# Optimization experiments

Measured on AMD Instinct MI355X. Metric: run time of the kernel, lower is better.

The kernel has to match this reference:

```python
import jax, jax.numpy as jnp
import numpy as np

N = 100000      # nodes
E = 1600000     # edges (avg degree 16)
IN = 128        # in_size
H = 4           # num_heads
DH = 16         # hid_size (per-head)
DO = 16         # out_size (per-head)
NEG_SLOPE = 0.2 # DGL GATConv default leaky_relu slope


def setup_inputs():
    key = jax.random.key(0)
    ks = jax.random.split(key, 12)
    s = 0.1
    return {
        "x":   jax.random.normal(ks[0], (N, IN), jnp.float32),
        "src": jax.random.randint(ks[1], (E,), 0, N, jnp.int32),
        "dst": jax.random.randint(ks[2], (E,), 0, N, jnp.int32),
        # layer 1: in=128 -> H*DH=64, residual Linear (128 != 64)
        "W1":    jax.random.normal(ks[3], (IN, H * DH), jnp.float32) * s,
        "al1":   jax.random.normal(ks[4], (H, DH), jnp.float32) * s,
        "ar1":   jax.random.normal(ks[5], (H, DH), jnp.float32) * s,
        "resW1": jax.random.normal(ks[6], (IN, H * DH), jnp.float32) * s,
        "b1":    jnp.zeros((H * DH,), jnp.float32),
        # layer 2: in=H*DH=64 -> H*DO=64, residual is Identity reshape (64 == 64)
        "W2":  jax.random.normal(ks[7], (H * DH, H * DO), jnp.float32) * s,
        "al2": jax.random.normal(ks[8], (H, DO), jnp.float32) * s,
        "ar2": jax.random.normal(ks[9], (H, DO), jnp.float32) * s,
        "b2":  jnp.zeros((H * DO,), jnp.float32),
    }


def gat_layer(h, W, al, ar, res, bias, src, dst):
    """One DGL-style GATConv (no internal activation). Returns [N, H, D]."""
    d = W.shape[1] // H
    feat = (h @ W).reshape(-1, H, d)                       # [N,H,D]
    el = jnp.einsum('nhd,hd->nh', feat, al)                # [N,H]
    er = jnp.einsum('nhd,hd->nh', feat, ar)                # [N,H]
    e = jax.nn.leaky_relu(el[src] + er[dst], NEG_SLOPE)    # [E,H]
    # segment softmax over incoming edges of each destination node
    emax = jax.lax.stop_gradient(jax.ops.segment_max(e, dst, num_segments=N))
    ee = jnp.exp(e - emax[dst])                            # [E,H]
    den = jax.ops.segment_sum(ee, dst, num_segments=N)     # [N,H]
    alpha = ee / den[dst]                                  # [E,H]
    msg = alpha[:, :, None] * feat[src]                    # [E,H,D]
    out = jax.ops.segment_sum(msg, dst, num_segments=N)    # [N,H,D]
    return out + res + bias.reshape(1, H, d)


def reference(x, src, dst, W1, al1, ar1, resW1, b1, W2, al2, ar2, b2):
    # layer 1 (residual via Linear since IN != H*DH)
    res1 = (x @ resW1).reshape(N, H, DH)
    h = gat_layer(x, W1, al1, ar1, res1, b1, src, dst)     # [N,H,DH]
    h = jax.nn.elu(h.reshape(N, H * DH))                   # flatten + elu (dropout=eval identity)
    # layer 2 (identity residual since H*DH == H*DO)
    res2 = h.reshape(N, H, DO)
    h = gat_layer(h, W2, al2, ar2, res2, b2, src, dst)     # [N,H,DO]
    return h.mean(axis=1)                                  # [N,DO]
```

## Files before the change

kernel.cpp:

```cpp
#include <hip/hip_runtime.h>
#include <hip/hip_bf16.h>

static inline int cdiv(int a, int b){ return (a+b-1)/b; }

#define LEAKY(x) ((x) >= 0.f ? (x) : 0.2f*(x))

#define NBK   256
#define NBKSH 8
#define CAP   5120
#define SCAP  1024

__device__ inline unsigned short bf16bits(float f){
  __hip_bfloat16 h = __float2bfloat16(f);
  return *reinterpret_cast<unsigned short*>(&h);
}


__global__ __launch_bounds__(256) void binA(const int* __restrict__ src,
    const int* __restrict__ dst, int* __restrict__ acur, unsigned int* __restrict__ tmp,
    int E, int B, int epb)
{
  __shared__ int cnt1[512], cnt2[512], gbase[512];
  const int tid = threadIdx.x;
  for (int j = tid; j < 512; j += 256) { cnt1[j] = 0; cnt2[j] = 0; }
  __syncthreads();
  const int beg = blockIdx.x*epb, end = min(E, beg+epb);
  for (int e = beg+tid; e < end; e += 256) atomicAdd(&cnt1[dst[e]>>NBKSH], 1);
  __syncthreads();
  for (int j = tid; j < B; j += 256) gbase[j] = atomicAdd(&acur[j], cnt1[j]);
  __syncthreads();
  for (int e = beg+tid; e < end; e += 256) {
    int s = src[e], d = dst[e];
    int b = d >> NBKSH;
    int tk = atomicAdd(&cnt2[b], 1);
    int slot = gbase[b] + tk;
    if (slot < CAP)
      tmp[(size_t)b*CAP + slot] = ((unsigned)s << NBKSH) | (unsigned)(d & (NBK-1));
  }
}


__global__ __launch_bounds__(512) void bucket_scan(const int* __restrict__ acur,
    int* __restrict__ bbase, int* __restrict__ off, int B, int N, int E)
{
  __shared__ int wsum[8];
  const int tid = threadIdx.x, lane = tid & 63, wave = tid >> 6;
  int v = (tid < B) ? acur[tid] : 0;
  int x = v;
  #pragma unroll
  for (int s = 1; s < 64; s <<= 1) { int t = __shfl_up(x, s); if (lane >= s) x += t; }
  if (lane == 63) wsum[wave] = x;
  __syncthreads();
  if (tid == 0) { int r = 0; for (int w = 0; w < 8; w++) { int t = wsum[w]; wsum[w] = r; r += t; } }
  __syncthreads();
  int excl = wsum[wave] + x - v;
  if (tid < B)    bbase[tid] = excl;
  if (tid == B-1) bbase[B]   = excl + v;
  if (tid == 0)   off[N]     = E;
}


__global__ __launch_bounds__(256) void binC(const unsigned int* __restrict__ tmp,
    const int* __restrict__ acur, const int* __restrict__ bbase,
    int* __restrict__ off, int* __restrict__ csr_src, int N)
{
  __shared__ int sA[NBK], sB[NBK];
  const int b = blockIdx.x, tid = threadIdx.x;
  const int m = min(acur[b], CAP);
  const int base = bbase[b];
  const int n0 = b*NBK;
  const int nn = min(NBK, N - n0);
  if (tid < NBK) sA[tid] = 0;
  __syncthreads();
  const unsigned int* tb = tmp + (size_t)b*CAP;
  for (int i = tid; i < m; i += 256) atomicAdd(&sA[tb[i] & (NBK-1)], 1);
  __syncthreads();
  int* in = sA; int* ob = sB;
  for (int st = 1; st < NBK; st <<= 1) {
    if (tid < NBK) { int v = in[tid]; if (tid >= st) v += in[tid-st]; ob[tid] = v; }
    __syncthreads();
    int* t = in; in = ob; ob = t;
  }
  if (tid < NBK) ob[tid] = tid ? in[tid-1] : 0;
  __syncthreads();
  if (tid < nn) off[n0 + tid] = base + ob[tid];
  __syncthreads();
  for (int i = tid; i < m; i += 256) {
    unsigned v = tb[i];
    int pos = atomicAdd(&ob[v & (NBK-1)], 1);
    csr_src[base + pos] = (int)(v >> NBKSH);
  }
}


__global__ __launch_bounds__(256) void lin128_once(const float* __restrict__ X,
    const float* __restrict__ W, const float* __restrict__ RW,
    const float* __restrict__ al, const float* __restrict__ ar,
    unsigned short* __restrict__ featb, float* __restrict__ el, float* __restrict__ er,
    float* __restrict__ res, int n)
{
  __shared__ float Ws[128*64];
  __shared__ float Xs[32*129];
  const int tid = threadIdx.x;
  const int nbase = blockIdx.x * 32;
  for (int i = tid; i < 128*64/4; i += 256) ((float4*)Ws)[i] = ((const float4*)W)[i];
  for (int idx = tid; idx < 32*32; idx += 256) {
    int node = idx >> 5, fq = idx & 31;
    int gn = nbase + node;
    float4 v = (gn < n) ? ((const float4*)X)[(size_t)gn*32 + fq] : float4{0.f,0.f,0.f,0.f};
    Xs[node*129 + fq*4 + 0] = v.x;
    Xs[node*129 + fq*4 + 1] = v.y;
    Xs[node*129 + fq*4 + 2] = v.z;
    Xs[node*129 + fq*4 + 3] = v.w;
  }
  __syncthreads();
  const int c0 = (tid & 15) * 4;
  const int n0 = (tid >> 4) * 2;
  const int g0 = nbase + n0, g1 = g0 + 1;
  {
    float a00=0,a01=0,a02=0,a03=0, a10=0,a11=0,a12=0,a13=0;
    #pragma unroll 4
    for (int k = 0; k < 128; k++) {
      float4 w = *(const float4*)&Ws[k*64 + c0];
      float x0 = Xs[n0*129 + k];
      float x1 = Xs[n0*129 + 129 + k];
      a00 = fmaf(x0, w.x, a00); a01 = fmaf(x0, w.y, a01);
      a02 = fmaf(x0, w.z, a02); a03 = fmaf(x0, w.w, a03);
      a10 = fmaf(x1, w.x, a10); a11 = fmaf(x1, w.y, a11);
      a12 = fmaf(x1, w.z, a12); a13 = fmaf(x1, w.w, a13);
    }
    if (g0 < n) *(ushort4*)&featb[(size_t)g0*64 + c0] = ushort4{bf16bits(a00),bf16bits(a01),bf16bits(a02),bf16bits(a03)};
    if (g1 < n) *(ushort4*)&featb[(size_t)g1*64 + c0] = ushort4{bf16bits(a10),bf16bits(a11),bf16bits(a12),bf16bits(a13)};
    float l0=al[c0], l1=al[c0+1], l2=al[c0+2], l3=al[c0+3];
    float r0=ar[c0], r1=ar[c0+1], r2=ar[c0+2], r3=ar[c0+3];
    float e0 = a00*l0 + a01*l1 + a02*l2 + a03*l3;
    float e1 = a10*l0 + a11*l1 + a12*l2 + a13*l3;
    float q0 = a00*r0 + a01*r1 + a02*r2 + a03*r3;
    float q1 = a10*r0 + a11*r1 + a12*r2 + a13*r3;
    e0 += __shfl_xor(e0,1); e0 += __shfl_xor(e0,2);
    e1 += __shfl_xor(e1,1); e1 += __shfl_xor(e1,2);
    q0 += __shfl_xor(q0,1); q0 += __shfl_xor(q0,2);
    q1 += __shfl_xor(q1,1); q1 += __shfl_xor(q1,2);
    if ((tid & 3) == 0) {
      int h = (tid & 15) >> 2;
      if (g0 < n) { el[g0*4+h] = e0; er[g0*4+h] = q0; }
      if (g1 < n) { el[g1*4+h] = e1; er[g1*4+h] = q1; }
    }
  }
  __syncthreads();
  for (int i = tid; i < 128*64/4; i += 256) ((float4*)Ws)[i] = ((const float4*)RW)[i];
  __syncthreads();
  {
    float a00=0,a01=0,a02=0,a03=0, a10=0,a11=0,a12=0,a13=0;
    #pragma unroll 4
    for (int k = 0; k < 128; k++) {
      float4 w = *(const float4*)&Ws[k*64 + c0];
      float x0 = Xs[n0*129 + k];
      float x1 = Xs[n0*129 + 129 + k];
      a00 = fmaf(x0, w.x, a00); a01 = fmaf(x0, w.y, a01);
      a02 = fmaf(x0, w.z, a02); a03 = fmaf(x0, w.w, a03);
      a10 = fmaf(x1, w.x, a10); a11 = fmaf(x1, w.y, a11);
      a12 = fmaf(x1, w.z, a12); a13 = fmaf(x1, w.w, a13);
    }
    if (g0 < n) *(float4*)&res[(size_t)g0*64 + c0] = float4{a00,a01,a02,a03};
    if (g1 < n) *(float4*)&res[(size_t)g1*64 + c0] = float4{a10,a11,a12,a13};
  }
}


__global__ __launch_bounds__(256) void lin64(const float* __restrict__ X,
    const float* __restrict__ W, const float* __restrict__ al, const float* __restrict__ ar,
    unsigned short* __restrict__ feat, float* __restrict__ el, float* __restrict__ er, int n)
{
  __shared__ float Ws[64*64];
  __shared__ float Xs[64*65];
  const int tid = threadIdx.x;
  const int nbase = blockIdx.x * 64;
  for (int i = tid; i < 64*64/4; i += 256) ((float4*)Ws)[i] = ((const float4*)W)[i];
  for (int idx = tid; idx < 64*16; idx += 256) {
    int node = idx >> 4, fq = idx & 15;
    int gn = nbase + node;
    float4 v = (gn < n) ? ((const float4*)X)[(size_t)gn*16 + fq] : float4{0.f,0.f,0.f,0.f};
    Xs[node*65 + fq*4 + 0] = v.x;
    Xs[node*65 + fq*4 + 1] = v.y;
    Xs[node*65 + fq*4 + 2] = v.z;
    Xs[node*65 + fq*4 + 3] = v.w;
  }
  __syncthreads();
  const int c0 = (tid & 15) * 4;
  const int n0 = (tid >> 4) * 4;
  float acc[4][4];
  #pragma unroll
  for (int i = 0; i < 4; i++)
    #pragma unroll
    for (int j = 0; j < 4; j++) acc[i][j] = 0.f;
  #pragma unroll 4
  for (int k = 0; k < 64; k++) {
    float4 w = *(const float4*)&Ws[k*64 + c0];
    #pragma unroll
    for (int i = 0; i < 4; i++) {
      float x = Xs[(n0+i)*65 + k];
      acc[i][0] = fmaf(x, w.x, acc[i][0]);
      acc[i][1] = fmaf(x, w.y, acc[i][1]);
      acc[i][2] = fmaf(x, w.z, acc[i][2]);
      acc[i][3] = fmaf(x, w.w, acc[i][3]);
    }
  }
  float l0=al[c0], l1=al[c0+1], l2=al[c0+2], l3=al[c0+3];
  float r0=ar[c0], r1=ar[c0+1], r2=ar[c0+2], r3=ar[c0+3];
  #pragma unroll
  for (int i = 0; i < 4; i++) {
    int g = nbase + n0 + i;
    if (g < n) *(ushort4*)&feat[(size_t)g*64 + c0] =
        ushort4{bf16bits(acc[i][0]),bf16bits(acc[i][1]),bf16bits(acc[i][2]),bf16bits(acc[i][3])};
    float e = acc[i][0]*l0 + acc[i][1]*l1 + acc[i][2]*l2 + acc[i][3]*l3;
    float q = acc[i][0]*r0 + acc[i][1]*r1 + acc[i][2]*r2 + acc[i][3]*r3;
    e += __shfl_xor(e,1); e += __shfl_xor(e,2);
    q += __shfl_xor(q,1); q += __shfl_xor(q,2);
    if ((tid & 3) == 0 && g < n) {
      int h = (tid & 15) >> 2;
      el[g*4+h] = e; er[g*4+h] = q;
    }
  }
}


template<int LAYER>
__global__ __launch_bounds__(256) void aggregate_fused(const int* __restrict__ off,
    const int* __restrict__ csr_src, const float* __restrict__ el, const float* __restrict__ er,
    const __hip_bfloat16* __restrict__ feat, const float* __restrict__ res,
    const float* __restrict__ bias, float* __restrict__ out, int n)
{
  __shared__ float sp[SCAP*4];
  __shared__ float er_s[4][4];
  __shared__ int   so[5];
  const int tid = threadIdx.x, wave = tid >> 6, lane = tid & 63;
  const int nb = blockIdx.x*4;
  if (tid < 5) so[tid] = off[min(nb + tid, n)];
  if (tid >= 5 && tid < 21) {
    int t = tid - 5;
    int g = nb + (t >> 2);
    er_s[t >> 2][t & 3] = (g < n) ? er[g*4 + (t & 3)] : 0.f;
  }
  __syncthreads();
  const int b0 = so[0], b4 = so[4];
  const int cnt = b4 - b0;
  const bool staged = cnt <= SCAP;
  if (staged) {
    const int o1 = so[1], o2 = so[2], o3 = so[3];
    for (int j = b0 + tid; j < b4; j += 256) {
      int s = csr_src[j];
      int t = (j >= o1) + (j >= o2) + (j >= o3);
      float4 l = *(const float4*)&el[s*4];
      int li = j - b0;
      sp[li*4+0] = __expf(LEAKY(l.x + er_s[t][0]));
      sp[li*4+1] = __expf(LEAKY(l.y + er_s[t][1]));
      sp[li*4+2] = __expf(LEAKY(l.z + er_s[t][2]));
      sp[li*4+3] = __expf(LEAKY(l.w + er_s[t][3]));
    }
  }
  __syncthreads();
  const int node = nb + wave;
  if (node >= n) return;
  const int h = lane >> 4;
  const int beg = so[wave], end = so[wave+1];
  float d[8], a[8];
  #pragma unroll
  for (int k = 0; k < 8; k++) { d[k] = 0.f; a[k] = 0.f; }
  int i = beg;
  if (staged) {
    for (; i + 8 <= end; i += 8) {
      int   s[8]; float p[8], f[8];
      #pragma unroll
      for (int k = 0; k < 8; k++) s[k] = csr_src[i+k];
      #pragma unroll
      for (int k = 0; k < 8; k++) p[k] = sp[(i+k-b0)*4 + h];
      #pragma unroll
      for (int k = 0; k < 8; k++) f[k] = __bfloat162float(feat[(size_t)s[k]*64 + lane]);
      #pragma unroll
      for (int k = 0; k < 8; k++) { d[k] += p[k]; a[k] = fmaf(p[k], f[k], a[k]); }
    }
    for (; i < end; i++) {
      int s = csr_src[i];
      float p = sp[(i-b0)*4 + h];
      d[0] += p;
      a[0] = fmaf(p, __bfloat162float(feat[(size_t)s*64 + lane]), a[0]);
    }
  } else {
    const float erh = er_s[wave][h];
    for (; i < end; i++) {
      int s = csr_src[i];
      float p = __expf(LEAKY(el[s*4 + h] + erh));
      d[0] += p;
      a[0] = fmaf(p, __bfloat162float(feat[(size_t)s*64 + lane]), a[0]);
    }
  }
  float den = ((d[0]+d[1])+(d[2]+d[3])) + ((d[4]+d[5])+(d[6]+d[7]));
  float acc = ((a[0]+a[1])+(a[2]+a[3])) + ((a[4]+a[5])+(a[6]+a[7]));
  float v = (den > 0.f) ? (acc/den) : 0.f;
  v += res[(size_t)node*64 + lane] + bias[lane];
  if (LAYER == 1) {
    v = (v > 0.f) ? v : expm1f(v);
    out[(size_t)node*64 + lane] = v;
  } else {
    v += __shfl_xor(v, 16);
    v += __shfl_xor(v, 32);
    if (lane < 16) out[(size_t)node*16 + lane] = 0.25f*v;
  }
}


extern "C" void kernel_launch(void* const* d_in, const int* in_sizes, int n_in,
                              void* d_out, int out_size, void* d_ws, size_t ws_size,
                              hipStream_t stream)
{
  (void)n_in; (void)out_size; (void)ws_size;
  const float* x   = (const float*)d_in[0];
  const int*   src = (const int*)  d_in[1];
  const int*   dst = (const int*)  d_in[2];
  const float* W1  = (const float*)d_in[3];
  const float* al1 = (const float*)d_in[4];
  const float* ar1 = (const float*)d_in[5];
  const float* rW1 = (const float*)d_in[6];
  const float* b1  = (const float*)d_in[7];
  const float* W2  = (const float*)d_in[8];
  const float* al2 = (const float*)d_in[9];
  const float* ar2 = (const float*)d_in[10];
  const float* b2  = (const float*)d_in[11];
  float* out = (float*)d_out;

  const int N_ = in_sizes[0] / 128;
  const int E_ = in_sizes[1];
  const int B_ = cdiv(N_, NBK);

  char* ws = (char*)d_ws;
  size_t o = 0;
  auto alloc = [&](size_t bytes)->char* {
    char* p = ws + o; o += (bytes + 255) & ~(size_t)255; return p;
  };
  int*   acur    = (int*)  alloc((size_t)B_*4);
  int*   bbase   = (int*)  alloc(((size_t)B_+1)*4);
  int*   off     = (int*)  alloc(((size_t)N_+1)*4);
  unsigned int* tmp = (unsigned int*)alloc((size_t)B_*CAP*4);
  int*   csr_src = (int*)  alloc((size_t)E_*4);
  unsigned short* featb = (unsigned short*)alloc((size_t)N_*64*2);
  float* el      = (float*)alloc((size_t)N_*4*4);
  float* er      = (float*)alloc((size_t)N_*4*4);
  float* hbuf    = (float*)alloc((size_t)N_*64*4);

  hipMemsetAsync(acur, 0, (size_t)B_*4, stream);
  binA<<<256, 256, 0, stream>>>(src, dst, acur, tmp, E_, B_, cdiv(E_,256));
  bucket_scan<<<1, 512, 0, stream>>>(acur, bbase, off, B_, N_, E_);
  binC<<<B_, 256, 0, stream>>>(tmp, acur, bbase, off, csr_src, N_);

  lin128_once<<<cdiv(N_,32), 256, 0, stream>>>(x, W1, rW1, al1, ar1, featb, el, er, hbuf, N_);
  aggregate_fused<1><<<cdiv(N_,4), 256, 0, stream>>>(off, csr_src, el, er,
      (const __hip_bfloat16*)featb, hbuf, b1, hbuf, N_);

  lin64<<<cdiv(N_,64), 256, 0, stream>>>(hbuf, W2, al2, ar2, featb, el, er, N_);
  aggregate_fused<2><<<cdiv(N_,4), 256, 0, stream>>>(off, csr_src, el, er,
      (const __hip_bfloat16*)featb, hbuf, b2, out, N_);
}
```

Before: 406.8 us.

## Process four edges per wave with vectorized bf16 gathers in aggregation

The aggregation kernel now splits each 64-lane wave into four 16-lane groups, each handling a different edge and loading 4 bf16 features (8 bytes) per lane instead of one scalar bf16 per lane. Partial sums are combined with cross-group shuffles, and the epilogue writes float4 results from 16 lanes. This raises memory-level parallelism and cuts instruction count per gathered row, at the cost of extra shuffles and masked tail iterations. The shared staging capacity is also halved (SCAP 512), which lowers LDS use per block but sends more blocks to the unstaged fallback path.

```diff
diff --git a/kernel.cpp b/kernel.cpp
--- a/kernel.cpp
+++ b/kernel.cpp
@@ -8,12 +8,14 @@
 #define NBK   256
 #define NBKSH 8
 #define CAP   5120
-#define SCAP  1024
+#define SCAP  512
 
 __device__ inline unsigned short bf16bits(float f){
   __hip_bfloat16 h = __float2bfloat16(f);
   return *reinterpret_cast<unsigned short*>(&h);
 }
+__device__ inline float bf16lo(unsigned u){ return __uint_as_float(u << 16); }
+__device__ inline float bf16hi(unsigned u){ return __uint_as_float(u & 0xffff0000u); }
 
 
 __global__ __launch_bounds__(256) void binA(const int* __restrict__ src,
@@ -228,7 +230,7 @@
 template<int LAYER>
 __global__ __launch_bounds__(256) void aggregate_fused(const int* __restrict__ off,
     const int* __restrict__ csr_src, const float* __restrict__ el, const float* __restrict__ er,
-    const __hip_bfloat16* __restrict__ feat, const float* __restrict__ res,
+    const unsigned short* __restrict__ feat, const float* __restrict__ res,
     const float* __restrict__ bias, float* __restrict__ out, int n)
 {
   __shared__ float sp[SCAP*4];
@@ -244,8 +246,7 @@
   }
   __syncthreads();
   const int b0 = so[0], b4 = so[4];
-  const int cnt = b4 - b0;
-  const bool staged = cnt <= SCAP;
+  const bool staged = (b4 - b0) <= SCAP;
   if (staged) {
     const int o1 = so[1], o2 = so[2], o3 = so[3];
     for (int j = b0 + tid; j < b4; j += 256) {
@@ -262,50 +263,78 @@
   __syncthreads();
   const int node = nb + wave;
   if (node >= n) return;
-  const int h = lane >> 4;
+  const int q = lane & 15, eg = lane >> 4;
+  const int hq = q >> 2;
+  const unsigned qoff = (unsigned)q * 8u;
+  const char* fbase = (const char*)feat;
   const int beg = so[wave], end = so[wave+1];
-  float d[8], a[8];
-  #pragma unroll
-  for (int k = 0; k < 8; k++) { d[k] = 0.f; a[k] = 0.f; }
+  float ac0=0.f, ac1=0.f, ac2=0.f, ac3=0.f, dn0=0.f, dn1=0.f;
   int i = beg;
   if (staged) {
     for (; i + 8 <= end; i += 8) {
-      int   s[8]; float p[8], f[8];
-      #pragma unroll
-      for (int k = 0; k < 8; k++) s[k] = csr_src[i+k];
-      #pragma unroll
-      for (int k = 0; k < 8; k++) p[k] = sp[(i+k-b0)*4 + h];
-      #pragma unroll
-      for (int k = 0; k < 8; k++) f[k] = __bfloat162float(feat[(size_t)s[k]*64 + lane]);
-      #pragma unroll
-      for (int k = 0; k < 8; k++) { d[k] += p[k]; a[k] = fmaf(p[k], f[k], a[k]); }
-    }
-    for (; i < end; i++) {
-      int s = csr_src[i];
-      float p = sp[(i-b0)*4 + h];
-      d[0] += p;
-      a[0] = fmaf(p, __bfloat162float(feat[(size_t)s*64 + lane]), a[0]);
+      int e0 = i + eg, e1 = i + 4 + eg;
+      int s0 = csr_src[e0], s1 = csr_src[e1];
+      float p0 = sp[(e0 - b0)*4 + hq];
+      float p1 = sp[(e1 - b0)*4 + hq];
+      uint2 w0 = *(const uint2*)(fbase + (((unsigned)s0 << 7) + qoff));
+      uint2 w1 = *(const uint2*)(fbase + (((unsigned)s1 << 7) + qoff));
+      dn0 += p0; dn1 += p1;
+      ac0 = fmaf(p0, bf16lo(w0.x), ac0); ac1 = fmaf(p0, bf16hi(w0.x), ac1);
+      ac2 = fmaf(p0, bf16lo(w0.y), ac2); ac3 = fmaf(p0, bf16hi(w0.y), ac3);
+      ac0 = fmaf(p1, bf16lo(w1.x), ac0); ac1 = fmaf(p1, bf16hi(w1.x), ac1);
+      ac2 = fmaf(p1, bf16lo(w1.y), ac2); ac3 = fmaf(p1, bf16hi(w1.y), ac3);
+    }
+    for (; i < end; i += 4) {
+      int e = i + eg;
+      bool act = e < end;
+      int s = csr_src[act ? e : (end-1)];
+      float p = act ? sp[(e - b0)*4 + hq] : 0.f;
+      uint2 w = *(const uint2*)(fbase + (((unsigned)s << 7) + qoff));
+      dn0 += p;
+      ac0 = fmaf(p, bf16lo(w.x), ac0); ac1 = fmaf(p, bf16hi(w.x), ac1);
+      ac2 = fmaf(p, bf16lo(w.y), ac2); ac3 = fmaf(p, bf16hi(w.y), ac3);
     }
   } else {
-    const float erh = er_s[wave][h];
-    for (; i < end; i++) {
-      int s = csr_src[i];
-      float p = __expf(LEAKY(el[s*4 + h] + erh));
-      d[0] += p;
-      a[0] = fmaf(p, __bfloat162float(feat[(size_t)s*64 + lane]), a[0]);
-    }
-  }
-  float den = ((d[0]+d[1])+(d[2]+d[3])) + ((d[4]+d[5])+(d[6]+d[7]));
-  float acc = ((a[0]+a[1])+(a[2]+a[3])) + ((a[4]+a[5])+(a[6]+a[7]));
-  float v = (den > 0.f) ? (acc/den) : 0.f;
-  v += res[(size_t)node*64 + lane] + bias[lane];
-  if (LAYER == 1) {
-    v = (v > 0.f) ? v : expm1f(v);
-    out[(size_t)node*64 + lane] = v;
-  } else {
-    v += __shfl_xor(v, 16);
-    v += __shfl_xor(v, 32);
-    if (lane < 16) out[(size_t)node*16 + lane] = 0.25f*v;
+    const float erh = er_s[wave][hq];
+    for (; i < end; i += 4) {
+      int e = i + eg;
+      bool act = e < end;
+      int s = csr_src[act ? e : (end-1)];
+      float p = act ? __expf(LEAKY(el[s*4 + hq] + erh)) : 0.f;
+      uint2 w = *(const uint2*)(fbase + (((unsigned)s << 7) + qoff));
+      dn0 += p;
+      ac0 = fmaf(p, bf16lo(w.x), ac0); ac1 = fmaf(p, bf16hi(w.x), ac1);
+      ac2 = fmaf(p, bf16lo(w.y), ac2); ac3 = fmaf(p, bf16hi(w.y), ac3);
+    }
+  }
+  float den = dn0 + dn1;
+  ac0 += __shfl_xor(ac0,16); ac0 += __shfl_xor(ac0,32);
+  ac1 += __shfl_xor(ac1,16); ac1 += __shfl_xor(ac1,32);
+  ac2 += __shfl_xor(ac2,16); ac2 += __shfl_xor(ac2,32);
+  ac3 += __shfl_xor(ac3,16); ac3 += __shfl_xor(ac3,32);
+  den += __shfl_xor(den,16); den += __shfl_xor(den,32);
+  if (lane < 16) {
+    float inv = (den > 0.f) ? (1.0f/den) : 0.f;
+    const float4 rq = *(const float4*)&res[(size_t)node*64 + q*4];
+    const float4 bq = *(const float4*)&bias[q*4];
+    float v0 = ac0*inv + rq.x + bq.x;
+    float v1 = ac1*inv + rq.y + bq.y;
+    float v2 = ac2*inv + rq.z + bq.z;
+    float v3 = ac3*inv + rq.w + bq.w;
+    if (LAYER == 1) {
+      v0 = (v0 > 0.f) ? v0 : expm1f(v0);
+      v1 = (v1 > 0.f) ? v1 : expm1f(v1);
+      v2 = (v2 > 0.f) ? v2 : expm1f(v2);
+      v3 = (v3 > 0.f) ? v3 : expm1f(v3);
+      *(float4*)&out[(size_t)node*64 + q*4] = float4{v0,v1,v2,v3};
+    } else {
+      v0 += __shfl_xor(v0,4); v0 += __shfl_xor(v0,8);
+      v1 += __shfl_xor(v1,4); v1 += __shfl_xor(v1,8);
+      v2 += __shfl_xor(v2,4); v2 += __shfl_xor(v2,8);
+      v3 += __shfl_xor(v3,4); v3 += __shfl_xor(v3,8);
+      if (q < 4)
+        *(float4*)&out[(size_t)node*16 + q*4] = float4{0.25f*v0,0.25f*v1,0.25f*v2,0.25f*v3};
+    }
   }
 }
 
@@ -355,9 +384,9 @@
 
   lin128_once<<<cdiv(N_,32), 256, 0, stream>>>(x, W1, rW1, al1, ar1, featb, el, er, hbuf, N_);
   aggregate_fused<1><<<cdiv(N_,4), 256, 0, stream>>>(off, csr_src, el, er,
-      (const __hip_bfloat16*)featb, hbuf, b1, hbuf, N_);
+      featb, hbuf, b1, hbuf, N_);
 
   lin64<<<cdiv(N_,64), 256, 0, stream>>>(hbuf, W2, al2, ar2, featb, el, er, N_);
   aggregate_fused<2><<<cdiv(N_,4), 256, 0, stream>>>(off, csr_src, el, er,
-      (const __hip_bfloat16*)featb, hbuf, b2, out, N_);
-}
+      featb, hbuf, b2, out, N_);
+}
```

Measured after the change: 368.8 us. -9.3%, faster.
